# Kernel optimization log

Measured on AMD Instinct MI355X. Metric: run time of the kernel, lower is better.

The kernel has to match this reference:

```python
import jax, jax.numpy as jnp
import numpy as np

B, L, SD, PD, H, HD, OH = 2, 256, 64, 32, 4, 16, 32
EXP = 64  # MBConv hidden = pair_dim * expand_ratio(2)
SE = 16   # squeezed channels = int(64 * 0.25)


def _ln(x, g, b, eps=1e-5):
    m = jnp.mean(x, -1, keepdims=True)
    v = jnp.mean((x - m) ** 2, -1, keepdims=True)
    return (x - m) / jnp.sqrt(v + eps) * g + b


def _inorm(x, eps=1e-5):  # InstanceNorm2d (no affine), x: [B,C,H,W]
    m = jnp.mean(x, (2, 3), keepdims=True)
    v = jnp.mean((x - m) ** 2, (2, 3), keepdims=True)
    return (x - m) / jnp.sqrt(v + eps)


def setup_inputs() -> dict:
    key = jax.random.key(0)
    ks = jax.random.split(key, 16)
    s = jnp.float32(0.02)
    return dict(
        seq_repr=jax.random.normal(ks[0], (B, L, SD), jnp.float32),
        pair_repr=jax.random.normal(ks[1], (B, L, L, PD), jnp.float32),
        g_attn=jnp.ones((SD,), jnp.float32), b_attn=jnp.zeros((SD,), jnp.float32),
        g_pair=jnp.ones((PD,), jnp.float32), b_pair=jnp.zeros((PD,), jnp.float32),
        W_opm_lin=jax.random.normal(ks[2], (SD, OH), jnp.float32) * s,
        b_opm_lin=jnp.zeros((OH,), jnp.float32),
        g_opm=jnp.ones((OH * OH,), jnp.float32), b_opm=jnp.zeros((OH * OH,), jnp.float32),
        W_opm_proj=jax.random.normal(ks[3], (OH * OH, PD), jnp.float32) * s,
        b_opm_proj=jnp.zeros((PD,), jnp.float32),
        W_exp=jax.random.normal(ks[4], (EXP, PD), jnp.float32) * s,
        W_dw=jax.random.normal(ks[5], (EXP, 1, 3, 3), jnp.float32) * s,
        W_se1=jax.random.normal(ks[6], (SE, EXP), jnp.float32) * s,
        b_se1=jnp.zeros((SE,), jnp.float32),
        W_se2=jax.random.normal(ks[7], (EXP, SE), jnp.float32) * s,
        b_se2=jnp.zeros((EXP,), jnp.float32),
        W_pw=jax.random.normal(ks[8], (PD, EXP), jnp.float32) * s,
        W_qkv=jax.random.normal(ks[9], (SD, 3 * SD), jnp.float32) * s,
        W_outp=jax.random.normal(ks[10], (SD, SD), jnp.float32) * s,
        b_outp=jnp.zeros((SD,), jnp.float32),
        W_bias=jax.random.normal(ks[11], (PD, H), jnp.float32) * s,
    )


def reference(seq_repr, pair_repr, g_attn, b_attn, g_pair, b_pair,
              W_opm_lin, b_opm_lin, g_opm, b_opm, W_opm_proj, b_opm_proj,
              W_exp, W_dw, W_se1, b_se1, W_se2, b_se2, W_pw,
              W_qkv, W_outp, b_outp, W_bias):
    # --- OuterProductMean on attn_norm(seq) ---
    x = _ln(seq_repr, g_attn, b_attn)                            # [B,L,SD]
    a = x @ W_opm_lin + b_opm_lin                                # [B,L,OH]
    outer = jnp.einsum('bid,bje->bijde', a, a).reshape(B, L, L, OH * OH)
    op = _ln(outer, g_opm, b_opm) @ W_opm_proj + b_opm_proj      # [B,L,L,PD]
    pair = pair_repr + op
    # --- MBConv pair processor on pair_norm(pair) ---
    pn = _ln(pair, g_pair, b_pair)
    z0 = jnp.transpose(pn, (0, 3, 1, 2))                         # NCHW [B,PD,L,L]
    h = jax.nn.silu(_inorm(jnp.einsum('bcij,oc->boij', z0, W_exp)))
    h = jax.lax.conv_general_dilated(h, W_dw, (1, 1), 'SAME',
                                     feature_group_count=EXP,
                                     dimension_numbers=('NCHW', 'OIHW', 'NCHW'))
    h = jax.nn.silu(_inorm(h))
    sq = jnp.mean(h, (2, 3), keepdims=True)                      # squeeze [B,EXP,1,1]
    sq = jax.nn.silu(jnp.einsum('bcij,oc->boij', sq, W_se1) + b_se1[None, :, None, None])
    sq = jax.nn.sigmoid(jnp.einsum('bcij,oc->boij', sq, W_se2) + b_se2[None, :, None, None])
    h = h * sq
    h = _inorm(jnp.einsum('bcij,oc->boij', h, W_pw))             # project back to PD
    pair = pair + jnp.transpose(z0 + h, (0, 2, 3, 1))            # MBConv residual + outer residual
    # --- Pairwise-bias attention ---
    pn2 = _ln(pair, g_pair, b_pair)
    bias = jnp.einsum('bijp,ph->bhij', pn2, W_bias)              # [B,H,L,L]
    q, k, v = jnp.split(x @ W_qkv, 3, axis=-1)
    q = q.reshape(B, L, H, HD).transpose(0, 2, 1, 3)
    k = k.reshape(B, L, H, HD).transpose(0, 2, 1, 3)
    v = v.reshape(B, L, H, HD).transpose(0, 2, 1, 3)
    scores = jnp.einsum('bhid,bhjd->bhij', q, k) / jnp.sqrt(jnp.float32(HD)) + bias
    w = jax.nn.softmax(scores, axis=-1)
    ctx = jnp.einsum('bhij,bhjd->bhid', w, v).transpose(0, 2, 1, 3).reshape(B, L, SD)
    seq = seq_repr + ctx @ W_outp + b_outp
    return seq, pair
```

## Files before the change

kernel.cpp:

```cpp
#include <hip/hip_runtime.h>
#include <hip/hip_bf16.h>

#define LLSZ 65536
#define INV_LL (1.f / 65536.f)


__device__ __forceinline__ void chan_stats(const float* sum, const float* sumsq,
                                           int chan, float& m, float& isd)
{
    m = sum[chan] * INV_LL;
    float var = sumsq[chan] * INV_LL - m * m;
    isd = rsqrtf(var + 1e-5f);
}

__device__ __forceinline__ float silu(float t) { return t / (1.f + expf(-t)); }

__global__ __launch_bounds__(1024) void k0_prep(
    const float* __restrict__ g_opm, const float* __restrict__ b_opm,
    const float* __restrict__ Wproj, const float* __restrict__ b_proj,
    float* __restrict__ G, float* __restrict__ GW, float* __restrict__ BW)
{
    int tid = threadIdx.x;
    int p = tid & 31, rg = tid >> 5;
    float gw = 0.f, bw = 0.f;
    #pragma unroll 4
    for (int k = 0; k < 32; ++k) {
        int de = k * 32 + rg;
        float wv = Wproj[de * 32 + p];
        float gv = g_opm[de] * wv;
        G[de * 32 + p] = gv;
        gw += gv;
        bw += b_opm[de] * wv;
    }
    __shared__ float rG[1024], rB[1024];
    rG[rg * 32 + p] = gw;
    rB[rg * 32 + p] = bw;
    __syncthreads();
    for (int s = 16; s > 0; s >>= 1) {
        if (rg < s) {
            rG[rg * 32 + p] += rG[(rg + s) * 32 + p];
            rB[rg * 32 + p] += rB[(rg + s) * 32 + p];
        }
        __syncthreads();
    }
    if (tid < 32) { GW[p] = rG[p]; BW[p] = rB[p] + b_proj[p]; }
}

__global__ __launch_bounds__(256) void k1_seq(
    const float* __restrict__ seq, const float* __restrict__ g_attn,
    const float* __restrict__ b_attn, const float* __restrict__ W_lin,
    const float* __restrict__ b_lin, const float* __restrict__ W_qkv,
    float* __restrict__ a, float* __restrict__ am, float* __restrict__ s2,
    float* __restrict__ qkv)
{
    __shared__ float Wq[64 * 192];
    __shared__ float Wl[64 * 32];
    __shared__ float xL[4][64];
    int tid = threadIdx.x;
    #pragma unroll
    for (int k = 0; k < 48; ++k) Wq[k * 256 + tid] = W_qkv[k * 256 + tid];
    #pragma unroll
    for (int k = 0; k < 8; ++k) Wl[k * 256 + tid] = W_lin[k * 256 + tid];

    int sub = tid >> 6, t = tid & 63;
    int row = blockIdx.x * 4 + sub;
    float v = seq[row * 64 + t];
    float m = v;
    for (int k = 32; k > 0; k >>= 1) m += __shfl_xor(m, k, 64);
    m *= (1.f / 64.f);
    float d = v - m;
    float var = d * d;
    for (int k = 32; k > 0; k >>= 1) var += __shfl_xor(var, k, 64);
    var *= (1.f / 64.f);
    float x = d * rsqrtf(var + 1e-5f) * g_attn[t] + b_attn[t];
    xL[sub][t] = x;
    __syncthreads();

    if (t < 32) {
        float s = 0.f;
        #pragma unroll
        for (int dd = 0; dd < 64; ++dd) s += xL[sub][dd] * Wl[dd * 32 + t];
        s += b_lin[t];
        a[row * 32 + t] = s;
        float mm = s, ss = s * s;
        for (int k = 16; k > 0; k >>= 1) {
            mm += __shfl_xor(mm, k, 32);
            ss += __shfl_xor(ss, k, 32);
        }
        if (t == 0) { am[row] = mm * (1.f / 32.f); s2[row] = ss * (1.f / 32.f); }
    }
    #pragma unroll
    for (int c3 = 0; c3 < 3; ++c3) {
        int c = c3 * 64 + t;
        float s = 0.f;
        #pragma unroll
        for (int dd = 0; dd < 64; ++dd) s += xL[sub][dd] * Wq[dd * 192 + c];
        qkv[row * 192 + c] = s;
    }
}

__global__ __launch_bounds__(256) void k2_T(
    const float* __restrict__ a, const float* __restrict__ G, float* __restrict__ T)
{
    int row = blockIdx.x;
    int tid = threadIdx.x;
    __shared__ float aL[32];
    if (tid < 32) aL[tid] = a[row * 32 + tid];
    __syncthreads();
    for (int k = 0; k < 4; ++k) {
        int idx = k * 256 + tid;
        float s = 0.f;
        #pragma unroll
        for (int d = 0; d < 32; ++d) s += aL[d] * G[d * 1024 + idx];
        T[row * 1024 + idx] = s;
    }
}

__global__ __launch_bounds__(256) void k3_op(
    const float* __restrict__ a, const float* __restrict__ am,
    const float* __restrict__ s2, const float* __restrict__ T,
    const float* __restrict__ GW, const float* __restrict__ BW,
    const float* __restrict__ pair_in, float* __restrict__ pair1)
{
    int blk = blockIdx.x;
    int row = blk >> 3;
    int jg = blk & 7;
    int b = row >> 8;
    int j0 = jg * 32;
    int tid = threadIdx.x;
    __shared__ float Tl[1024];
    __shared__ float aL[32 * 33];
    __shared__ float amL[32], s2L[32], gwL[32], bwL[32];
    ((float4*)Tl)[tid] = ((const float4*)(T + (long)row * 1024))[tid];
    for (int k = 0; k < 4; ++k) {
        int idx = k * 256 + tid;
        aL[(idx >> 5) * 33 + (idx & 31)] = a[(b * 256 + j0) * 32 + idx];
    }
    if (tid < 32) {
        amL[tid] = am[b * 256 + j0 + tid];
        s2L[tid] = s2[b * 256 + j0 + tid];
        gwL[tid] = GW[tid];
        bwL[tid] = BW[tid];
    }
    __syncthreads();
    int jl = tid >> 3, cq = tid & 7;
    float am_i = am[row], s2_i = s2[row];
    float m = am_i * amL[jl];
    float isd = rsqrtf(s2_i * s2L[jl] - m * m + 1e-5f);
    long base = ((long)row * 256 + j0 + jl) * 32 + cq * 4;
    float4 pv = *(const float4*)(pair_in + base);
    float o[4];
    #pragma unroll
    for (int u = 0; u < 4; ++u) {
        int p = cq * 4 + u;
        float S = 0.f;
        #pragma unroll
        for (int e = 0; e < 32; ++e) S += aL[jl * 33 + e] * Tl[e * 32 + p];
        o[u] = isd * (S - m * gwL[p]) + bwL[p];
    }
    pv.x += o[0]; pv.y += o[1]; pv.z += o[2]; pv.w += o[3];
    *(float4*)(pair1 + base) = pv;
}

__global__ __launch_bounds__(256) void k4_expand(
    const float* __restrict__ pair1, const float* __restrict__ g_pair,
    const float* __restrict__ b_pair, const float* __restrict__ W_exp,
    float* __restrict__ e1)
{
    int blk = blockIdx.x;
    int b = blk >> 9;
    int pixbase = (blk & 511) * 128;
    int tid = threadIdx.x;
    __shared__ float pnL[128 * 33];
    __shared__ float We[2048];
    __shared__ float gL[32], bL[32];
    for (int k = 0; k < 8; ++k) We[k * 256 + tid] = W_exp[k * 256 + tid];
    if (tid < 32) { gL[tid] = g_pair[tid]; bL[tid] = b_pair[tid]; }
    const float4* src = (const float4*)(pair1 + ((long)b * LLSZ + pixbase) * 32);
    for (int k = 0; k < 4; ++k) {
        int idx = k * 256 + tid;
        int pix = idx >> 3, cq = idx & 7;
        float4 v = src[idx];
        pnL[pix * 33 + cq * 4 + 0] = v.x;
        pnL[pix * 33 + cq * 4 + 1] = v.y;
        pnL[pix * 33 + cq * 4 + 2] = v.z;
        pnL[pix * 33 + cq * 4 + 3] = v.w;
    }
    __syncthreads();
    int pix = tid & 127, og = tid >> 7;
    float s = 0.f, q = 0.f;
    #pragma unroll
    for (int c = 0; c < 32; ++c) { float v = pnL[pix * 33 + c]; s += v; q += v * v; }
    float mu = s * (1.f / 32.f);
    float isd = rsqrtf(q * (1.f / 32.f) - mu * mu + 1e-5f);
    float x[32];
    #pragma unroll
    for (int c = 0; c < 32; ++c) x[c] = (pnL[pix * 33 + c] - mu) * isd * gL[c] + bL[c];
    for (int oo = 0; oo < 32; ++oo) {
        int o = og * 32 + oo;
        float acc = 0.f;
        #pragma unroll
        for (int c = 0; c < 32; ++c) acc += x[c] * We[o * 32 + c];
        e1[((long)(b * 64 + o)) * LLSZ + pixbase + pix] = acc;
    }
}

__global__ __launch_bounds__(256) void k_stats(
    const float* __restrict__ buf, float* __restrict__ sum, float* __restrict__ sumsq)
{
    int bid = blockIdx.x;
    int chan = bid >> 3, seg = bid & 7;
    int tid = threadIdx.x;
    const float4* p = (const float4*)(buf + (long)chan * LLSZ + seg * 8192);
    float s = 0.f, ss = 0.f;
    #pragma unroll
    for (int k = 0; k < 8; ++k) {
        float4 v = p[k * 256 + tid];
        s += v.x + v.y + v.z + v.w;
        ss += v.x * v.x + v.y * v.y + v.z * v.z + v.w * v.w;
    }
    for (int k = 32; k > 0; k >>= 1) { s += __shfl_xor(s, k, 64); ss += __shfl_xor(ss, k, 64); }
    __shared__ float rs[4], rq[4];
    int wave = tid >> 6;
    if ((tid & 63) == 0) { rs[wave] = s; rq[wave] = ss; }
    __syncthreads();
    if (tid == 0) {
        atomicAdd(&sum[chan], rs[0] + rs[1] + rs[2] + rs[3]);
        atomicAdd(&sumsq[chan], rq[0] + rq[1] + rq[2] + rq[3]);
    }
}

__global__ __launch_bounds__(256) void k6_dw(
    const float* __restrict__ e1, const float* __restrict__ st1s,
    const float* __restrict__ st1q, const float* __restrict__ W_dw,
    float* __restrict__ h2)
{
    int blk = blockIdx.x;
    int chan = blk >> 5;
    int r0 = (blk & 31) * 8;
    int o = chan & 63;
    int tid = threadIdx.x;
    float m, isd;
    chan_stats(st1s, st1q, chan, m, isd);
    __shared__ float sL[10][258];
    const float* src = e1 + (long)chan * LLSZ;
    for (int k = tid; k < 640; k += 256) {
        int rr = k >> 6, c4 = k & 63;
        int g = r0 - 1 + rr;
        float4 v = make_float4(0.f, 0.f, 0.f, 0.f);
        if (g >= 0 && g < 256) v = *(const float4*)(src + g * 256 + c4 * 4);
        float t;
        t = (v.x - m) * isd; v.x = (g >= 0 && g < 256) ? silu(t) : 0.f;
        t = (v.y - m) * isd; v.y = (g >= 0 && g < 256) ? silu(t) : 0.f;
        t = (v.z - m) * isd; v.z = (g >= 0 && g < 256) ? silu(t) : 0.f;
        t = (v.w - m) * isd; v.w = (g >= 0 && g < 256) ? silu(t) : 0.f;
        sL[rr][1 + c4 * 4 + 0] = v.x;
        sL[rr][1 + c4 * 4 + 1] = v.y;
        sL[rr][1 + c4 * 4 + 2] = v.z;
        sL[rr][1 + c4 * 4 + 3] = v.w;
    }
    if (tid < 10) { sL[tid][0] = 0.f; sL[tid][257] = 0.f; }
    float w[9];
    #pragma unroll
    for (int k = 0; k < 9; ++k) w[k] = W_dw[o * 9 + k];
    __syncthreads();
    int c = tid;
    #pragma unroll
    for (int rr = 0; rr < 8; ++rr) {
        float s = 0.f;
        #pragma unroll
        for (int ki = 0; ki < 3; ++ki)
            #pragma unroll
            for (int kj = 0; kj < 3; ++kj)
                s += sL[rr + ki][c + kj] * w[ki * 3 + kj];
        h2[(long)chan * LLSZ + (r0 + rr) * 256 + c] = s;
    }
}

__global__ __launch_bounds__(256) void k8_squeeze(
    const float* __restrict__ h2, const float* __restrict__ st2s,
    const float* __restrict__ st2q, float* __restrict__ sqs)
{
    int bid = blockIdx.x;
    int chan = bid >> 3, seg = bid & 7;
    int tid = threadIdx.x;
    float m, isd;
    chan_stats(st2s, st2q, chan, m, isd);
    const float4* p = (const float4*)(h2 + (long)chan * LLSZ + seg * 8192);
    float s = 0.f;
    #pragma unroll
    for (int k = 0; k < 8; ++k) {
        float4 v = p[k * 256 + tid];
        s += silu((v.x - m) * isd) + silu((v.y - m) * isd)
           + silu((v.z - m) * isd) + silu((v.w - m) * isd);
    }
    for (int k = 32; k > 0; k >>= 1) s += __shfl_xor(s, k, 64);
    __shared__ float rs[4];
    int wave = tid >> 6;
    if ((tid & 63) == 0) rs[wave] = s;
    __syncthreads();
    if (tid == 0) atomicAdd(&sqs[chan], rs[0] + rs[1] + rs[2] + rs[3]);
}

__global__ __launch_bounds__(256) void k10_pw(
    const float* __restrict__ h2, const float* __restrict__ st2s,
    const float* __restrict__ st2q, const float* __restrict__ sqs,
    const float* __restrict__ W_se1, const float* __restrict__ b_se1,
    const float* __restrict__ W_se2, const float* __restrict__ b_se2,
    const float* __restrict__ W_pw, float* __restrict__ hp,
    float* __restrict__ st3s, float* __restrict__ st3q)
{
    int blk = blockIdx.x;
    int b = blk >> 8;
    int pixbase = (blk & 255) * 256;
    int tid = threadIdx.x;
    __shared__ float hL[32 * 256];
    __shared__ float Wp[2048];
    __shared__ float s1L[16];
    __shared__ float sqvL[64];
    __shared__ float red[4][32], redq[4][32];
    for (int k = 0; k < 8; ++k) Wp[k * 256 + tid] = W_pw[k * 256 + tid];
    if (tid < 16) {
        float s = 0.f;
        for (int c = 0; c < 64; ++c) s += sqs[b * 64 + c] * W_se1[tid * 64 + c];
        s = s * INV_LL + b_se1[tid];
        s1L[tid] = silu(s);
    }
    __syncthreads();
    if (tid < 64) {
        float s = 0.f;
        #pragma unroll
        for (int j = 0; j < 16; ++j) s += s1L[j] * W_se2[tid * 16 + j];
        s += b_se2[tid];
        sqvL[tid] = 1.f / (1.f + expf(-s));
    }
    float acc[32];
    #pragma unroll
    for (int p = 0; p < 32; ++p) acc[p] = 0.f;
    for (int half = 0; half < 2; ++half) {
        __syncthreads();
        for (int k = 0; k < 8; ++k) {
            int idx = k * 256 + tid;
            int c = idx >> 6, q4 = idx & 63;
            int chan = b * 64 + half * 32 + c;
            float m, isd;
            chan_stats(st2s, st2q, chan, m, isd);
            float sc = sqvL[half * 32 + c];
            float4 v = *(const float4*)(h2 + (long)chan * LLSZ + pixbase + q4 * 4);
            v.x = silu((v.x - m) * isd) * sc;
            v.y = silu((v.y - m) * isd) * sc;
            v.z = silu((v.z - m) * isd) * sc;
            v.w = silu((v.w - m) * isd) * sc;
            *(float4*)(hL + c * 256 + q4 * 4) = v;
        }
        __syncthreads();
        #pragma unroll
        for (int p = 0; p < 32; ++p) {
            float s = 0.f;
            #pragma unroll
            for (int c = 0; c < 32; ++c) s += hL[c * 256 + tid] * Wp[p * 64 + half * 32 + c];
            acc[p] += s;
        }
    }
    int wave = tid >> 6, lane = tid & 63;
    #pragma unroll
    for (int p = 0; p < 32; ++p) {
        float v = acc[p];
        hp[((long)(b * 32 + p)) * LLSZ + pixbase + tid] = v;
        float s = v, q = v * v;
        for (int k = 32; k > 0; k >>= 1) { s += __shfl_xor(s, k, 64); q += __shfl_xor(q, k, 64); }
        if (lane == 0) { red[wave][p] = s; redq[wave][p] = q; }
    }
    __syncthreads();
    if (tid < 32) {
        atomicAdd(&st3s[b * 32 + tid], red[0][tid] + red[1][tid] + red[2][tid] + red[3][tid]);
        atomicAdd(&st3q[b * 32 + tid], redq[0][tid] + redq[1][tid] + redq[2][tid] + redq[3][tid]);
    }
}

__global__ __launch_bounds__(256) void k12_merge(
    const float* __restrict__ pair1, const float* __restrict__ hp,
    const float* __restrict__ st3s, const float* __restrict__ st3q,
    const float* __restrict__ g_pair, const float* __restrict__ b_pair,
    const float* __restrict__ W_bias, float* __restrict__ pair_out,
    float* __restrict__ biasbuf)
{
    int blk = blockIdx.x;
    int b = blk >> 8;
    int pixbase = (blk & 255) * 256;
    int tid = threadIdx.x;
    __shared__ float hpL[32][257];
    for (int k = 0; k < 8; ++k) {
        int idx = k * 256 + tid;
        int p = idx >> 6, q4 = idx & 63;
        int chan = b * 32 + p;
        float m, isd;
        chan_stats(st3s, st3q, chan, m, isd);
        float4 v = *(const float4*)(hp + (long)chan * LLSZ + pixbase + q4 * 4);
        hpL[p][q4 * 4 + 0] = (v.x - m) * isd;
        hpL[p][q4 * 4 + 1] = (v.y - m) * isd;
        hpL[p][q4 * 4 + 2] = (v.z - m) * isd;
        hpL[p][q4 * 4 + 3] = (v.w - m) * isd;
    }
    __syncthreads();
    int pg = tid >> 3, cq = tid & 7;
    float gp[4], bp[4], wb[4][4];
    #pragma unroll
    for (int u = 0; u < 4; ++u) {
        int c = cq * 4 + u;
        gp[u] = g_pair[c]; bp[u] = b_pair[c];
        #pragma unroll
        for (int h = 0; h < 4; ++h) wb[u][h] = W_bias[c * 4 + h];
    }
    for (int it = 0; it < 8; ++it) {
        int pix = it * 32 + pg;
        long base = ((long)b * LLSZ + pixbase + pix) * 32;
        float4 v1 = *(const float4*)(pair1 + base + cq * 4);
        float s = v1.x + v1.y + v1.z + v1.w;
        float q = v1.x * v1.x + v1.y * v1.y + v1.z * v1.z + v1.w * v1.w;
        s += __shfl_xor(s, 1, 8); q += __shfl_xor(q, 1, 8);
        s += __shfl_xor(s, 2, 8); q += __shfl_xor(q, 2, 8);
        s += __shfl_xor(s, 4, 8); q += __shfl_xor(q, 4, 8);
        float mu = s * (1.f / 32.f);
        float isd = rsqrtf(q * (1.f / 32.f) - mu * mu + 1e-5f);
        float vo[4], vv1[4] = {v1.x, v1.y, v1.z, v1.w};
        #pragma unroll
        for (int u = 0; u < 4; ++u) {
            float pnv = (vv1[u] - mu) * isd * gp[u] + bp[u];
            vo[u] = vv1[u] + pnv + hpL[cq * 4 + u][pix];
        }
        float4 vout = make_float4(vo[0], vo[1], vo[2], vo[3]);
        *(float4*)(pair_out + base + cq * 4) = vout;
        float s2_ = vo[0] + vo[1] + vo[2] + vo[3];
        float q2 = vo[0] * vo[0] + vo[1] * vo[1] + vo[2] * vo[2] + vo[3] * vo[3];
        s2_ += __shfl_xor(s2_, 1, 8); q2 += __shfl_xor(q2, 1, 8);
        s2_ += __shfl_xor(s2_, 2, 8); q2 += __shfl_xor(q2, 2, 8);
        s2_ += __shfl_xor(s2_, 4, 8); q2 += __shfl_xor(q2, 4, 8);
        float mu2 = s2_ * (1.f / 32.f);
        float isd2 = rsqrtf(q2 * (1.f / 32.f) - mu2 * mu2 + 1e-5f);
        float t[4] = {0.f, 0.f, 0.f, 0.f};
        #pragma unroll
        for (int u = 0; u < 4; ++u) {
            float pn2 = (vo[u] - mu2) * isd2 * gp[u] + bp[u];
            #pragma unroll
            for (int h = 0; h < 4; ++h) t[h] += pn2 * wb[u][h];
        }
        #pragma unroll
        for (int h = 0; h < 4; ++h) {
            t[h] += __shfl_xor(t[h], 1, 8);
            t[h] += __shfl_xor(t[h], 2, 8);
            t[h] += __shfl_xor(t[h], 4, 8);
        }
        if (cq == 0) {
            #pragma unroll
            for (int h = 0; h < 4; ++h)
                biasbuf[((long)(b * 4 + h)) * LLSZ + pixbase + pix] = t[h];
        }
    }
}

__global__ __launch_bounds__(256) void k13_attn(
    const float* __restrict__ qkv, const float* __restrict__ biasbuf,
    float* __restrict__ ctx)
{
    int blk = blockIdx.x;
    int b = blk >> 8;
    int h = (blk >> 6) & 3;
    int ig = blk & 63;
    int wave = threadIdx.x >> 6, lane = threadIdx.x & 63;
    int i = ig * 4 + wave;
    const float* qrow = qkv + ((long)(b * 256 + i)) * 192 + h * 16;
    float qv[16];
    #pragma unroll
    for (int d = 0; d < 16; ++d) qv[d] = qrow[d];
    float sj[4];
    #pragma unroll
    for (int q = 0; q < 4; ++q) {
        int j = lane + 64 * q;
        const float* kr = qkv + ((long)(b * 256 + j)) * 192 + 64 + h * 16;
        float s = 0.f;
        #pragma unroll
        for (int d = 0; d < 16; ++d) s += qv[d] * kr[d];
        sj[q] = s * 0.25f + biasbuf[((long)(b * 4 + h)) * LLSZ + i * 256 + j];
    }
    float mx = fmaxf(fmaxf(sj[0], sj[1]), fmaxf(sj[2], sj[3]));
    for (int k = 32; k > 0; k >>= 1) mx = fmaxf(mx, __shfl_xor(mx, k, 64));
    float wgt[4], wsum = 0.f;
    #pragma unroll
    for (int q = 0; q < 4; ++q) { wgt[q] = expf(sj[q] - mx); wsum += wgt[q]; }
    for (int k = 32; k > 0; k >>= 1) wsum += __shfl_xor(wsum, k, 64);
    float inv = 1.f / wsum;
    float o[16];
    #pragma unroll
    for (int d = 0; d < 16; ++d) o[d] = 0.f;
    #pragma unroll
    for (int q = 0; q < 4; ++q) {
        const float* vr = qkv + ((long)(b * 256 + lane + 64 * q)) * 192 + 128 + h * 16;
        #pragma unroll
        for (int d = 0; d < 16; ++d) o[d] += wgt[q] * vr[d];
    }
    #pragma unroll
    for (int d = 0; d < 16; ++d)
        for (int k = 32; k > 0; k >>= 1) o[d] += __shfl_xor(o[d], k, 64);
    if (lane == 0) {
        #pragma unroll
        for (int d = 0; d < 16; ++d)
            ctx[((long)(b * 256 + i)) * 64 + h * 16 + d] = o[d] * inv;
    }
}

__global__ __launch_bounds__(256) void k14_seqout(
    const float* __restrict__ seq, const float* __restrict__ ctx,
    const float* __restrict__ W_outp, const float* __restrict__ b_outp,
    float* __restrict__ out)
{
    __shared__ float Wo[64 * 64];
    __shared__ float cL[4][64];
    int tid = threadIdx.x;
    #pragma unroll
    for (int k = 0; k < 16; ++k) Wo[k * 256 + tid] = W_outp[k * 256 + tid];
    int sub = tid >> 6, t = tid & 63;
    int row = blockIdx.x * 4 + sub;
    cL[sub][t] = ctx[row * 64 + t];
    __syncthreads();
    float s = b_outp[t];
    #pragma unroll
    for (int u = 0; u < 64; ++u) s += cL[sub][u] * Wo[u * 64 + t];
    out[row * 64 + t] = seq[row * 64 + t] + s;
}

extern "C" void kernel_launch(void* const* d_in, const int* in_sizes, int n_in,
                              void* d_out, int out_size, void* d_ws, size_t ws_size,
                              hipStream_t stream) {
    const float* seq_repr   = (const float*)d_in[0];
    const float* pair_repr  = (const float*)d_in[1];
    const float* g_attn     = (const float*)d_in[2];
    const float* b_attn     = (const float*)d_in[3];
    const float* g_pair     = (const float*)d_in[4];
    const float* b_pair     = (const float*)d_in[5];
    const float* W_opm_lin  = (const float*)d_in[6];
    const float* b_opm_lin  = (const float*)d_in[7];
    const float* g_opm      = (const float*)d_in[8];
    const float* b_opm      = (const float*)d_in[9];
    const float* W_opm_proj = (const float*)d_in[10];
    const float* b_opm_proj = (const float*)d_in[11];
    const float* W_exp      = (const float*)d_in[12];
    const float* W_dw       = (const float*)d_in[13];
    const float* W_se1      = (const float*)d_in[14];
    const float* b_se1      = (const float*)d_in[15];
    const float* W_se2      = (const float*)d_in[16];
    const float* b_se2      = (const float*)d_in[17];
    const float* W_pw       = (const float*)d_in[18];
    const float* W_qkv      = (const float*)d_in[19];
    const float* W_outp     = (const float*)d_in[20];
    const float* b_outp     = (const float*)d_in[21];
    const float* W_bias     = (const float*)d_in[22];

    float* out_seq  = (float*)d_out;
    float* out_pair = (float*)d_out + 32768;

    float* w = (float*)d_ws;
    float* a_buf   = w;
    float* am_buf  = a_buf + 16384;
    float* s2_buf  = am_buf + 512;
    float* qkv_buf = s2_buf + 512;
    float* G_buf   = qkv_buf + 98304;
    float* GW_buf  = G_buf + 32768;
    float* BW_buf  = GW_buf + 32;
    float* ctx     = BW_buf + 32;
    float* st1s    = ctx + 32768;
    float* st1q    = st1s + 128;
    float* st2s    = st1q + 128;
    float* st2q    = st2s + 128;
    float* st3s    = st2q + 128;
    float* st3q    = st3s + 64;
    float* sqs     = st3q + 64;
    float* T_buf   = sqs + 128;
    float* biasb   = T_buf;
    float* pair1   = T_buf + 524288;
    float* e1      = pair1 + 4194304;
    float* hp      = e1;
    float* h2      = e1 + 8388608;

    hipMemsetAsync(st1s, 0, 768 * sizeof(float), stream);

    hipLaunchKernelGGL(k0_prep, dim3(1), dim3(1024), 0, stream,
                       g_opm, b_opm, W_opm_proj, b_opm_proj, G_buf, GW_buf, BW_buf);
    hipLaunchKernelGGL(k1_seq, dim3(128), dim3(256), 0, stream,
                       seq_repr, g_attn, b_attn, W_opm_lin, b_opm_lin, W_qkv,
                       a_buf, am_buf, s2_buf, qkv_buf);
    hipLaunchKernelGGL(k2_T, dim3(512), dim3(256), 0, stream, a_buf, G_buf, T_buf);
    hipLaunchKernelGGL(k3_op, dim3(4096), dim3(256), 0, stream,
                       a_buf, am_buf, s2_buf, T_buf, GW_buf, BW_buf,
                       pair_repr, pair1);
    hipLaunchKernelGGL(k4_expand, dim3(1024), dim3(256), 0, stream,
                       pair1, g_pair, b_pair, W_exp, e1);
    hipLaunchKernelGGL(k_stats, dim3(1024), dim3(256), 0, stream, e1, st1s, st1q);
    hipLaunchKernelGGL(k6_dw, dim3(4096), dim3(256), 0, stream,
                       e1, st1s, st1q, W_dw, h2);
    hipLaunchKernelGGL(k_stats, dim3(1024), dim3(256), 0, stream, h2, st2s, st2q);
    hipLaunchKernelGGL(k8_squeeze, dim3(1024), dim3(256), 0, stream,
                       h2, st2s, st2q, sqs);
    hipLaunchKernelGGL(k10_pw, dim3(512), dim3(256), 0, stream,
                       h2, st2s, st2q, sqs, W_se1, b_se1, W_se2, b_se2,
                       W_pw, hp, st3s, st3q);
    hipLaunchKernelGGL(k12_merge, dim3(512), dim3(256), 0, stream,
                       pair1, hp, st3s, st3q, g_pair, b_pair, W_bias,
                       out_pair, biasb);
    hipLaunchKernelGGL(k13_attn, dim3(512), dim3(256), 0, stream,
                       qkv_buf, biasb, ctx);
    hipLaunchKernelGGL(k14_seqout, dim3(128), dim3(256), 0, stream,
                       seq_repr, ctx, W_outp, b_outp, out_seq);
}
```

Baseline: 282.7 us.

## Fuse channel statistics into producers, merge prep kernels, shrink tiles for more blocks

The prep and sequence kernels are merged into one launch, and the memset is folded into that launch. The two standalone instance-norm statistics passes are removed: the expand kernel and the depthwise kernel now accumulate their per-channel sums and sums of squares with wave shuffles and atomics as they produce values. The expand, pointwise and merge kernels use smaller pixel tiles with more blocks, and the pointwise kernel's inner loop is reorganised into a register-blocked loop over all 64 channels. The aim is fewer launches and fewer full re-reads of large intermediates, at the cost of more atomics and some redundant per-block weight loads.

After: 337.2 us. 19.3% more time.

```diff
diff --git a/kernel.cpp b/kernel.cpp
--- a/kernel.cpp
+++ b/kernel.cpp
@@ -15,87 +15,85 @@
 
 __device__ __forceinline__ float silu(float t) { return t / (1.f + expf(-t)); }
 
-__global__ __launch_bounds__(1024) void k0_prep(
+__global__ __launch_bounds__(256) void kA(
     const float* __restrict__ g_opm, const float* __restrict__ b_opm,
     const float* __restrict__ Wproj, const float* __restrict__ b_proj,
-    float* __restrict__ G, float* __restrict__ GW, float* __restrict__ BW)
-{
-    int tid = threadIdx.x;
-    int p = tid & 31, rg = tid >> 5;
-    float gw = 0.f, bw = 0.f;
-    #pragma unroll 4
-    for (int k = 0; k < 32; ++k) {
-        int de = k * 32 + rg;
-        float wv = Wproj[de * 32 + p];
-        float gv = g_opm[de] * wv;
-        G[de * 32 + p] = gv;
-        gw += gv;
-        bw += b_opm[de] * wv;
-    }
-    __shared__ float rG[1024], rB[1024];
-    rG[rg * 32 + p] = gw;
-    rB[rg * 32 + p] = bw;
-    __syncthreads();
-    for (int s = 16; s > 0; s >>= 1) {
-        if (rg < s) {
-            rG[rg * 32 + p] += rG[(rg + s) * 32 + p];
-            rB[rg * 32 + p] += rB[(rg + s) * 32 + p];
-        }
-        __syncthreads();
-    }
-    if (tid < 32) { GW[p] = rG[p]; BW[p] = rB[p] + b_proj[p]; }
-}
-
-__global__ __launch_bounds__(256) void k1_seq(
+    float* __restrict__ G, float* __restrict__ GW, float* __restrict__ BW,
+    float* __restrict__ stats0,
     const float* __restrict__ seq, const float* __restrict__ g_attn,
     const float* __restrict__ b_attn, const float* __restrict__ W_lin,
     const float* __restrict__ b_lin, const float* __restrict__ W_qkv,
     float* __restrict__ a, float* __restrict__ am, float* __restrict__ s2,
     float* __restrict__ qkv)
 {
-    __shared__ float Wq[64 * 192];
-    __shared__ float Wl[64 * 32];
-    __shared__ float xL[4][64];
-    int tid = threadIdx.x;
-    #pragma unroll
-    for (int k = 0; k < 48; ++k) Wq[k * 256 + tid] = W_qkv[k * 256 + tid];
-    #pragma unroll
-    for (int k = 0; k < 8; ++k) Wl[k * 256 + tid] = W_lin[k * 256 + tid];
-
-    int sub = tid >> 6, t = tid & 63;
-    int row = blockIdx.x * 4 + sub;
-    float v = seq[row * 64 + t];
-    float m = v;
-    for (int k = 32; k > 0; k >>= 1) m += __shfl_xor(m, k, 64);
-    m *= (1.f / 64.f);
-    float d = v - m;
-    float var = d * d;
-    for (int k = 32; k > 0; k >>= 1) var += __shfl_xor(var, k, 64);
-    var *= (1.f / 64.f);
-    float x = d * rsqrtf(var + 1e-5f) * g_attn[t] + b_attn[t];
-    xL[sub][t] = x;
-    __syncthreads();
-
-    if (t < 32) {
-        float s = 0.f;
-        #pragma unroll
-        for (int dd = 0; dd < 64; ++dd) s += xL[sub][dd] * Wl[dd * 32 + t];
-        s += b_lin[t];
-        a[row * 32 + t] = s;
-        float mm = s, ss = s * s;
-        for (int k = 16; k > 0; k >>= 1) {
-            mm += __shfl_xor(mm, k, 32);
-            ss += __shfl_xor(ss, k, 32);
+    int tid = threadIdx.x;
+    if (blockIdx.x == 0) {
+        for (int k = tid; k < 768; k += 256) stats0[k] = 0.f;
+        int p = tid & 31, rg = tid >> 5;
+        float gw = 0.f, bw = 0.f;
+        #pragma unroll 8
+        for (int k = 0; k < 128; ++k) {
+            int de = k * 8 + rg;
+            float wv = Wproj[de * 32 + p];
+            float gv = g_opm[de] * wv;
+            G[de * 32 + p] = gv;
+            gw += gv;
+            bw += b_opm[de] * wv;
         }
-        if (t == 0) { am[row] = mm * (1.f / 32.f); s2[row] = ss * (1.f / 32.f); }
-    }
-    #pragma unroll
-    for (int c3 = 0; c3 < 3; ++c3) {
-        int c = c3 * 64 + t;
-        float s = 0.f;
-        #pragma unroll
-        for (int dd = 0; dd < 64; ++dd) s += xL[sub][dd] * Wq[dd * 192 + c];
-        qkv[row * 192 + c] = s;
+        __shared__ float rG[256], rB[256];
+        rG[rg * 32 + p] = gw;
+        rB[rg * 32 + p] = bw;
+        __syncthreads();
+        for (int s = 4; s > 0; s >>= 1) {
+            if (rg < s) {
+                rG[rg * 32 + p] += rG[(rg + s) * 32 + p];
+                rB[rg * 32 + p] += rB[(rg + s) * 32 + p];
+            }
+            __syncthreads();
+        }
+        if (tid < 32) { GW[p] = rG[p]; BW[p] = rB[p] + b_proj[p]; }
+    } else {
+        __shared__ float Wq[64 * 192];
+        __shared__ float Wl[64 * 32];
+        __shared__ float xL[4][64];
+        #pragma unroll
+        for (int k = 0; k < 48; ++k) Wq[k * 256 + tid] = W_qkv[k * 256 + tid];
+        #pragma unroll
+        for (int k = 0; k < 8; ++k) Wl[k * 256 + tid] = W_lin[k * 256 + tid];
+        int sub = tid >> 6, t = tid & 63;
+        int row = (blockIdx.x - 1) * 4 + sub;
+        float v = seq[row * 64 + t];
+        float m = v;
+        for (int k = 32; k > 0; k >>= 1) m += __shfl_xor(m, k, 64);
+        m *= (1.f / 64.f);
+        float d = v - m;
+        float var = d * d;
+        for (int k = 32; k > 0; k >>= 1) var += __shfl_xor(var, k, 64);
+        var *= (1.f / 64.f);
+        float x = d * rsqrtf(var + 1e-5f) * g_attn[t] + b_attn[t];
+        xL[sub][t] = x;
+        __syncthreads();
+        if (t < 32) {
+            float s = 0.f;
+            #pragma unroll
+            for (int dd = 0; dd < 64; ++dd) s += xL[sub][dd] * Wl[dd * 32 + t];
+            s += b_lin[t];
+            a[row * 32 + t] = s;
+            float mm = s, ss = s * s;
+            for (int k = 16; k > 0; k >>= 1) {
+                mm += __shfl_xor(mm, k, 32);
+                ss += __shfl_xor(ss, k, 32);
+            }
+            if (t == 0) { am[row] = mm * (1.f / 32.f); s2[row] = ss * (1.f / 32.f); }
+        }
+        #pragma unroll
+        for (int c3 = 0; c3 < 3; ++c3) {
+            int c = c3 * 64 + t;
+            float s = 0.f;
+            #pragma unroll
+            for (int dd = 0; dd < 64; ++dd) s += xL[sub][dd] * Wq[dd * 192 + c];
+            qkv[row * 192 + c] = s;
+        }
     }
 }
 
@@ -165,75 +163,68 @@
 __global__ __launch_bounds__(256) void k4_expand(
     const float* __restrict__ pair1, const float* __restrict__ g_pair,
     const float* __restrict__ b_pair, const float* __restrict__ W_exp,
-    float* __restrict__ e1)
+    float* __restrict__ e1, float* __restrict__ st1s, float* __restrict__ st1q)
 {
     int blk = blockIdx.x;
-    int b = blk >> 9;
-    int pixbase = (blk & 511) * 128;
-    int tid = threadIdx.x;
-    __shared__ float pnL[128 * 33];
+    int b = blk >> 10;
+    int pixbase = (blk & 1023) * 64;
+    int tid = threadIdx.x;
+    __shared__ float xL[64 * 33];
     __shared__ float We[2048];
+    __shared__ float muL[64], isdL[64];
     __shared__ float gL[32], bL[32];
     for (int k = 0; k < 8; ++k) We[k * 256 + tid] = W_exp[k * 256 + tid];
     if (tid < 32) { gL[tid] = g_pair[tid]; bL[tid] = b_pair[tid]; }
     const float4* src = (const float4*)(pair1 + ((long)b * LLSZ + pixbase) * 32);
-    for (int k = 0; k < 4; ++k) {
+    #pragma unroll
+    for (int k = 0; k < 2; ++k) {
         int idx = k * 256 + tid;
+        float4 v = src[idx];
         int pix = idx >> 3, cq = idx & 7;
-        float4 v = src[idx];
-        pnL[pix * 33 + cq * 4 + 0] = v.x;
-        pnL[pix * 33 + cq * 4 + 1] = v.y;
-        pnL[pix * 33 + cq * 4 + 2] = v.z;
-        pnL[pix * 33 + cq * 4 + 3] = v.w;
-    }
-    __syncthreads();
-    int pix = tid & 127, og = tid >> 7;
-    float s = 0.f, q = 0.f;
-    #pragma unroll
-    for (int c = 0; c < 32; ++c) { float v = pnL[pix * 33 + c]; s += v; q += v * v; }
-    float mu = s * (1.f / 32.f);
-    float isd = rsqrtf(q * (1.f / 32.f) - mu * mu + 1e-5f);
-    float x[32];
-    #pragma unroll
-    for (int c = 0; c < 32; ++c) x[c] = (pnL[pix * 33 + c] - mu) * isd * gL[c] + bL[c];
-    for (int oo = 0; oo < 32; ++oo) {
-        int o = og * 32 + oo;
+        xL[pix * 33 + cq * 4 + 0] = v.x;
+        xL[pix * 33 + cq * 4 + 1] = v.y;
+        xL[pix * 33 + cq * 4 + 2] = v.z;
+        xL[pix * 33 + cq * 4 + 3] = v.w;
+    }
+    __syncthreads();
+    if (tid < 64) {
+        float s = 0.f, q = 0.f;
+        #pragma unroll
+        for (int c = 0; c < 32; ++c) { float v = xL[tid * 33 + c]; s += v; q += v * v; }
+        float mu = s * (1.f / 32.f);
+        muL[tid] = mu;
+        isdL[tid] = rsqrtf(q * (1.f / 32.f) - mu * mu + 1e-5f);
+    }
+    __syncthreads();
+    #pragma unroll
+    for (int k = 0; k < 8; ++k) {
+        int idx = k * 256 + tid;
+        int pix = idx >> 5, c = idx & 31;
+        xL[pix * 33 + c] = (xL[pix * 33 + c] - muL[pix]) * isdL[pix] * gL[c] + bL[c];
+    }
+    __syncthreads();
+    int pix = tid & 63, og = tid >> 6;
+    float ssk = 0.f, qqk = 0.f;
+    for (int oo = 0; oo < 16; ++oo) {
+        int o = og * 16 + oo;
         float acc = 0.f;
         #pragma unroll
-        for (int c = 0; c < 32; ++c) acc += x[c] * We[o * 32 + c];
+        for (int c = 0; c < 32; ++c) acc += xL[pix * 33 + c] * We[o * 32 + c];
         e1[((long)(b * 64 + o)) * LLSZ + pixbase + pix] = acc;
-    }
-}
-
-__global__ __launch_bounds__(256) void k_stats(
-    const float* __restrict__ buf, float* __restrict__ sum, float* __restrict__ sumsq)
-{
-    int bid = blockIdx.x;
-    int chan = bid >> 3, seg = bid & 7;
-    int tid = threadIdx.x;
-    const float4* p = (const float4*)(buf + (long)chan * LLSZ + seg * 8192);
-    float s = 0.f, ss = 0.f;
-    #pragma unroll
-    for (int k = 0; k < 8; ++k) {
-        float4 v = p[k * 256 + tid];
-        s += v.x + v.y + v.z + v.w;
-        ss += v.x * v.x + v.y * v.y + v.z * v.z + v.w * v.w;
-    }
-    for (int k = 32; k > 0; k >>= 1) { s += __shfl_xor(s, k, 64); ss += __shfl_xor(ss, k, 64); }
-    __shared__ float rs[4], rq[4];
-    int wave = tid >> 6;
-    if ((tid & 63) == 0) { rs[wave] = s; rq[wave] = ss; }
-    __syncthreads();
-    if (tid == 0) {
-        atomicAdd(&sum[chan], rs[0] + rs[1] + rs[2] + rs[3]);
-        atomicAdd(&sumsq[chan], rq[0] + rq[1] + rq[2] + rq[3]);
+        float s = acc, q = acc * acc;
+        for (int k = 32; k > 0; k >>= 1) { s += __shfl_xor(s, k, 64); q += __shfl_xor(q, k, 64); }
+        if (pix == oo) { ssk = s; qqk = q; }
+    }
+    if (pix < 16) {
+        atomicAdd(&st1s[b * 64 + og * 16 + pix], ssk);
+        atomicAdd(&st1q[b * 64 + og * 16 + pix], qqk);
     }
 }
 
 __global__ __launch_bounds__(256) void k6_dw(
     const float* __restrict__ e1, const float* __restrict__ st1s,
     const float* __restrict__ st1q, const float* __restrict__ W_dw,
-    float* __restrict__ h2)
+    float* __restrict__ h2, float* __restrict__ st2s, float* __restrict__ st2q)
 {
     int blk = blockIdx.x;
     int chan = blk >> 5;
@@ -248,12 +239,13 @@
         int rr = k >> 6, c4 = k & 63;
         int g = r0 - 1 + rr;
         float4 v = make_float4(0.f, 0.f, 0.f, 0.f);
-        if (g >= 0 && g < 256) v = *(const float4*)(src + g * 256 + c4 * 4);
+        bool ok = (g >= 0 && g < 256);
+        if (ok) v = *(const float4*)(src + g * 256 + c4 * 4);
         float t;
-        t = (v.x - m) * isd; v.x = (g >= 0 && g < 256) ? silu(t) : 0.f;
-        t = (v.y - m) * isd; v.y = (g >= 0 && g < 256) ? silu(t) : 0.f;
-        t = (v.z - m) * isd; v.z = (g >= 0 && g < 256) ? silu(t) : 0.f;
-        t = (v.w - m) * isd; v.w = (g >= 0 && g < 256) ? silu(t) : 0.f;
+        t = (v.x - m) * isd; v.x = ok ? silu(t) : 0.f;
+        t = (v.y - m) * isd; v.y = ok ? silu(t) : 0.f;
+        t = (v.z - m) * isd; v.z = ok ? silu(t) : 0.f;
+        t = (v.w - m) * isd; v.w = ok ? silu(t) : 0.f;
         sL[rr][1 + c4 * 4 + 0] = v.x;
         sL[rr][1 + c4 * 4 + 1] = v.y;
         sL[rr][1 + c4 * 4 + 2] = v.z;
@@ -265,6 +257,7 @@
     for (int k = 0; k < 9; ++k) w[k] = W_dw[o * 9 + k];
     __syncthreads();
     int c = tid;
+    float bs = 0.f, bq = 0.f;
     #pragma unroll
     for (int rr = 0; rr < 8; ++rr) {
         float s = 0.f;
@@ -274,6 +267,16 @@
             for (int kj = 0; kj < 3; ++kj)
                 s += sL[rr + ki][c + kj] * w[ki * 3 + kj];
         h2[(long)chan * LLSZ + (r0 + rr) * 256 + c] = s;
+        bs += s; bq += s * s;
+    }
+    for (int k = 32; k > 0; k >>= 1) { bs += __shfl_xor(bs, k, 64); bq += __shfl_xor(bq, k, 64); }
+    __shared__ float r2s[4], r2q[4];
+    int wave = tid >> 6;
+    if ((tid & 63) == 0) { r2s[wave] = bs; r2q[wave] = bq; }
+    __syncthreads();
+    if (tid == 0) {
+        atomicAdd(&st2s[chan], r2s[0] + r2s[1] + r2s[2] + r2s[3]);
+        atomicAdd(&st2q[chan], r2q[0] + r2q[1] + r2q[2] + r2q[3]);
     }
 }
 
@@ -311,14 +314,13 @@
     float* __restrict__ st3s, float* __restrict__ st3q)
 {
     int blk = blockIdx.x;
-    int b = blk >> 8;
-    int pixbase = (blk & 255) * 256;
-    int tid = threadIdx.x;
-    __shared__ float hL[32 * 256];
+    int b = blk >> 10;
+    int pixbase = (blk & 1023) * 64;
+    int tid = threadIdx.x;
+    __shared__ float hL[64 * 65];
     __shared__ float Wp[2048];
     __shared__ float s1L[16];
     __shared__ float sqvL[64];
-    __shared__ float red[4][32], redq[4][32];
     for (int k = 0; k < 8; ++k) Wp[k * 256 + tid] = W_pw[k * 256 + tid];
     if (tid < 16) {
         float s = 0.f;
@@ -334,47 +336,45 @@
         s += b_se2[tid];
         sqvL[tid] = 1.f / (1.f + expf(-s));
     }
-    float acc[32];
-    #pragma unroll
-    for (int p = 0; p < 32; ++p) acc[p] = 0.f;
-    for (int half = 0; half < 2; ++half) {
-        __syncthreads();
-        for (int k = 0; k < 8; ++k) {
-            int idx = k * 256 + tid;
-            int c = idx >> 6, q4 = idx & 63;
-            int chan = b * 64 + half * 32 + c;
-            float m, isd;
-            chan_stats(st2s, st2q, chan, m, isd);
-            float sc = sqvL[half * 32 + c];
-            float4 v = *(const float4*)(h2 + (long)chan * LLSZ + pixbase + q4 * 4);
-            v.x = silu((v.x - m) * isd) * sc;
-            v.y = silu((v.y - m) * isd) * sc;
-            v.z = silu((v.z - m) * isd) * sc;
-            v.w = silu((v.w - m) * isd) * sc;
-            *(float4*)(hL + c * 256 + q4 * 4) = v;
-        }
-        __syncthreads();
-        #pragma unroll
-        for (int p = 0; p < 32; ++p) {
-            float s = 0.f;
-            #pragma unroll
-            for (int c = 0; c < 32; ++c) s += hL[c * 256 + tid] * Wp[p * 64 + half * 32 + c];
-            acc[p] += s;
-        }
-    }
-    int wave = tid >> 6, lane = tid & 63;
-    #pragma unroll
-    for (int p = 0; p < 32; ++p) {
-        float v = acc[p];
-        hp[((long)(b * 32 + p)) * LLSZ + pixbase + tid] = v;
+    __syncthreads();
+    #pragma unroll
+    for (int k = 0; k < 4; ++k) {
+        int idx = k * 256 + tid;
+        int c = idx >> 4, f4 = idx & 15;
+        int chan = b * 64 + c;
+        float m, isd;
+        chan_stats(st2s, st2q, chan, m, isd);
+        float sc = sqvL[c];
+        float4 v = *(const float4*)(h2 + (long)chan * LLSZ + pixbase + f4 * 4);
+        hL[c * 65 + f4 * 4 + 0] = silu((v.x - m) * isd) * sc;
+        hL[c * 65 + f4 * 4 + 1] = silu((v.y - m) * isd) * sc;
+        hL[c * 65 + f4 * 4 + 2] = silu((v.z - m) * isd) * sc;
+        hL[c * 65 + f4 * 4 + 3] = silu((v.w - m) * isd) * sc;
+    }
+    __syncthreads();
+    int pix = tid & 63, og = tid >> 6;
+    float acc[8];
+    #pragma unroll
+    for (int u = 0; u < 8; ++u) acc[u] = 0.f;
+    #pragma unroll
+    for (int c = 0; c < 64; ++c) {
+        float hv = hL[c * 65 + pix];
+        #pragma unroll
+        for (int u = 0; u < 8; ++u) acc[u] += hv * Wp[(og * 8 + u) * 64 + c];
+    }
+    float ssk = 0.f, qqk = 0.f;
+    #pragma unroll
+    for (int u = 0; u < 8; ++u) {
+        float v = acc[u];
+        int p = og * 8 + u;
+        hp[((long)(b * 32 + p)) * LLSZ + pixbase + pix] = v;
         float s = v, q = v * v;
         for (int k = 32; k > 0; k >>= 1) { s += __shfl_xor(s, k, 64); q += __shfl_xor(q, k, 64); }
-        if (lane == 0) { red[wave][p] = s; redq[wave][p] = q; }
-    }
-    __syncthreads();
-    if (tid < 32) {
-        atomicAdd(&st3s[b * 32 + tid], red[0][tid] + red[1][tid] + red[2][tid] + red[3][tid]);
-        atomicAdd(&st3q[b * 32 + tid], redq[0][tid] + redq[1][tid] + redq[2][tid] + redq[3][tid]);
+        if (pix == u) { ssk = s; qqk = q; }
+    }
+    if (pix < 8) {
+        atomicAdd(&st3s[b * 32 + og * 8 + pix], ssk);
+        atomicAdd(&st3q[b * 32 + og * 8 + pix], qqk);
     }
 }
 
@@ -386,21 +386,20 @@
     float* __restrict__ biasbuf)
 {
     int blk = blockIdx.x;
-    int b = blk >> 8;
-    int pixbase = (blk & 255) * 256;
-    int tid = threadIdx.x;
-    __shared__ float hpL[32][257];
-    for (int k = 0; k < 8; ++k) {
-        int idx = k * 256 + tid;
-        int p = idx >> 6, q4 = idx & 63;
-        int chan = b * 32 + p;
+    int b = blk >> 11;
+    int pixbase = (blk & 2047) * 32;
+    int tid = threadIdx.x;
+    __shared__ float hpL[32 * 33];
+    {
+        int c = tid >> 3, f4 = tid & 7;
+        int chan = b * 32 + c;
         float m, isd;
         chan_stats(st3s, st3q, chan, m, isd);
-        float4 v = *(const float4*)(hp + (long)chan * LLSZ + pixbase + q4 * 4);
-        hpL[p][q4 * 4 + 0] = (v.x - m) * isd;
-        hpL[p][q4 * 4 + 1] = (v.y - m) * isd;
-        hpL[p][q4 * 4 + 2] = (v.z - m) * isd;
-        hpL[p][q4 * 4 + 3] = (v.w - m) * isd;
+        float4 v = *(const float4*)(hp + (long)chan * LLSZ + pixbase + f4 * 4);
+        hpL[c * 33 + f4 * 4 + 0] = (v.x - m) * isd;
+        hpL[c * 33 + f4 * 4 + 1] = (v.y - m) * isd;
+        hpL[c * 33 + f4 * 4 + 2] = (v.z - m) * isd;
+        hpL[c * 33 + f4 * 4 + 3] = (v.w - m) * isd;
     }
     __syncthreads();
     int pg = tid >> 3, cq = tid & 7;
@@ -412,50 +411,47 @@
         #pragma unroll
         for (int h = 0; h < 4; ++h) wb[u][h] = W_bias[c * 4 + h];
     }
-    for (int it = 0; it < 8; ++it) {
-        int pix = it * 32 + pg;
-        long base = ((long)b * LLSZ + pixbase + pix) * 32;
-        float4 v1 = *(const float4*)(pair1 + base + cq * 4);
-        float s = v1.x + v1.y + v1.z + v1.w;
-        float q = v1.x * v1.x + v1.y * v1.y + v1.z * v1.z + v1.w * v1.w;
-        s += __shfl_xor(s, 1, 8); q += __shfl_xor(q, 1, 8);
-        s += __shfl_xor(s, 2, 8); q += __shfl_xor(q, 2, 8);
-        s += __shfl_xor(s, 4, 8); q += __shfl_xor(q, 4, 8);
-        float mu = s * (1.f / 32.f);
-        float isd = rsqrtf(q * (1.f / 32.f) - mu * mu + 1e-5f);
-        float vo[4], vv1[4] = {v1.x, v1.y, v1.z, v1.w};
-        #pragma unroll
-        for (int u = 0; u < 4; ++u) {
-            float pnv = (vv1[u] - mu) * isd * gp[u] + bp[u];
-            vo[u] = vv1[u] + pnv + hpL[cq * 4 + u][pix];
-        }
-        float4 vout = make_float4(vo[0], vo[1], vo[2], vo[3]);
-        *(float4*)(pair_out + base + cq * 4) = vout;
-        float s2_ = vo[0] + vo[1] + vo[2] + vo[3];
-        float q2 = vo[0] * vo[0] + vo[1] * vo[1] + vo[2] * vo[2] + vo[3] * vo[3];
-        s2_ += __shfl_xor(s2_, 1, 8); q2 += __shfl_xor(q2, 1, 8);
-        s2_ += __shfl_xor(s2_, 2, 8); q2 += __shfl_xor(q2, 2, 8);
-        s2_ += __shfl_xor(s2_, 4, 8); q2 += __shfl_xor(q2, 4, 8);
-        float mu2 = s2_ * (1.f / 32.f);
-        float isd2 = rsqrtf(q2 * (1.f / 32.f) - mu2 * mu2 + 1e-5f);
-        float t[4] = {0.f, 0.f, 0.f, 0.f};
-        #pragma unroll
-        for (int u = 0; u < 4; ++u) {
-            float pn2 = (vo[u] - mu2) * isd2 * gp[u] + bp[u];
-            #pragma unroll
-            for (int h = 0; h < 4; ++h) t[h] += pn2 * wb[u][h];
-        }
-        #pragma unroll
-        for (int h = 0; h < 4; ++h) {
-            t[h] += __shfl_xor(t[h], 1, 8);
-            t[h] += __shfl_xor(t[h], 2, 8);
-            t[h] += __shfl_xor(t[h], 4, 8);
-        }
-        if (cq == 0) {
-            #pragma unroll
-            for (int h = 0; h < 4; ++h)
-                biasbuf[((long)(b * 4 + h)) * LLSZ + pixbase + pix] = t[h];
-        }
+    int pix = pg;
+    long base = ((long)b * LLSZ + pixbase + pix) * 32;
+    float4 v1 = *(const float4*)(pair1 + base + cq * 4);
+    float s = v1.x + v1.y + v1.z + v1.w;
+    float q = v1.x * v1.x + v1.y * v1.y + v1.z * v1.z + v1.w * v1.w;
+    s += __shfl_xor(s, 1, 8); q += __shfl_xor(q, 1, 8);
+    s += __shfl_xor(s, 2, 8); q += __shfl_xor(q, 2, 8);
+    s += __shfl_xor(s, 4, 8); q += __shfl_xor(q, 4, 8);
+    float mu = s * (1.f / 32.f);
+    float isd = rsqrtf(q * (1.f / 32.f) - mu * mu + 1e-5f);
+    float vo[4], vv1[4] = {v1.x, v1.y, v1.z, v1.w};
+    #pragma unroll
+    for (int u = 0; u < 4; ++u) {
+        float pnv = (vv1[u] - mu) * isd * gp[u] + bp[u];
+        vo[u] = vv1[u] + pnv + hpL[(cq * 4 + u) * 33 + pix];
+    }
+    *(float4*)(pair_out + base + cq * 4) = make_float4(vo[0], vo[1], vo[2], vo[3]);
+    float s2_ = vo[0] + vo[1] + vo[2] + vo[3];
+    float q2 = vo[0] * vo[0] + vo[1] * vo[1] + vo[2] * vo[2] + vo[3] * vo[3];
+    s2_ += __shfl_xor(s2_, 1, 8); q2 += __shfl_xor(q2, 1, 8);
+    s2_ += __shfl_xor(s2_, 2, 8); q2 += __shfl_xor(q2, 2, 8);
+    s2_ += __shfl_xor(s2_, 4, 8); q2 += __shfl_xor(q2, 4, 8);
+    float mu2 = s2_ * (1.f / 32.f);
+    float isd2 = rsqrtf(q2 * (1.f / 32.f) - mu2 * mu2 + 1e-5f);
+    float t[4] = {0.f, 0.f, 0.f, 0.f};
+    #pragma unroll
+    for (int u = 0; u < 4; ++u) {
+        float pn2 = (vo[u] - mu2) * isd2 * gp[u] + bp[u];
+        #pragma unroll
+        for (int h = 0; h < 4; ++h) t[h] += pn2 * wb[u][h];
+    }
+    #pragma unroll
+    for (int h = 0; h < 4; ++h) {
+        t[h] += __shfl_xor(t[h], 1, 8);
+        t[h] += __shfl_xor(t[h], 2, 8);
+        t[h] += __shfl_xor(t[h], 4, 8);
+    }
+    if (cq == 0) {
+        #pragma unroll
+        for (int h = 0; h < 4; ++h)
+            biasbuf[((long)(b * 4 + h)) * LLSZ + pixbase + pix] = t[h];
     }
 }
 
@@ -582,29 +578,25 @@
     float* hp      = e1;
     float* h2      = e1 + 8388608;
 
-    hipMemsetAsync(st1s, 0, 768 * sizeof(float), stream);
-
-    hipLaunchKernelGGL(k0_prep, dim3(1), dim3(1024), 0, stream,
-                       g_opm, b_opm, W_opm_proj, b_opm_proj, G_buf, GW_buf, BW_buf);
-    hipLaunchKernelGGL(k1_seq, dim3(128), dim3(256), 0, stream,
+    hipLaunchKernelGGL(kA, dim3(129), dim3(256), 0, stream,
+                       g_opm, b_opm, W_opm_proj, b_opm_proj, G_buf, GW_buf, BW_buf,
+                       st1s,
                        seq_repr, g_attn, b_attn, W_opm_lin, b_opm_lin, W_qkv,
                        a_buf, am_buf, s2_buf, qkv_buf);
     hipLaunchKernelGGL(k2_T, dim3(512), dim3(256), 0, stream, a_buf, G_buf, T_buf);
     hipLaunchKernelGGL(k3_op, dim3(4096), dim3(256), 0, stream,
                        a_buf, am_buf, s2_buf, T_buf, GW_buf, BW_buf,
                        pair_repr, pair1);
-    hipLaunchKernelGGL(k4_expand, dim3(1024), dim3(256), 0, stream,
-                       pair1, g_pair, b_pair, W_exp, e1);
-    hipLaunchKernelGGL(k_stats, dim3(1024), dim3(256), 0, stream, e1, st1s, st1q);
+    hipLaunchKernelGGL(k4_expand, dim3(2048), dim3(256), 0, stream,
+                       pair1, g_pair, b_pair, W_exp, e1, st1s, st1q);
     hipLaunchKernelGGL(k6_dw, dim3(4096), dim3(256), 0, stream,
-                       e1, st1s, st1q, W_dw, h2);
-    hipLaunchKernelGGL(k_stats, dim3(1024), dim3(256), 0, stream, h2, st2s, st2q);
+                       e1, st1s, st1q, W_dw, h2, st2s, st2q);
     hipLaunchKernelGGL(k8_squeeze, dim3(1024), dim3(256), 0, stream,
                        h2, st2s, st2q, sqs);
-    hipLaunchKernelGGL(k10_pw, dim3(512), dim3(256), 0, stream,
+    hipLaunchKernelGGL(k10_pw, dim3(2048), dim3(256), 0, stream,
                        h2, st2s, st2q, sqs, W_se1, b_se1, W_se2, b_se2,
                        W_pw, hp, st3s, st3q);
-    hipLaunchKernelGGL(k12_merge, dim3(512), dim3(256), 0, stream,
+    hipLaunchKernelGGL(k12_merge, dim3(4096), dim3(256), 0, stream,
                        pair1, hp, st3s, st3q, g_pair, b_pair, W_bias,
                        out_pair, biasb);
     hipLaunchKernelGGL(k13_attn, dim3(512), dim3(256), 0, stream,
```
